# Performance work log

Hardware: AMD Instinct MI355X
Metric: run time of the kernel (lower is better)

The kernel has to match this reference:

```python
import jax, jax.numpy as jnp
import numpy as np

N_EMBED = 1024
HEAD_SIZE = 128
B, T = 8, 2048


def setup_inputs() -> dict:
    key = jax.random.key(0)
    kx, kk, kq, kv = jax.random.split(key, 4)
    x = jax.random.normal(kx, (B, T, N_EMBED), dtype=jnp.float32)
    Wk = jax.random.normal(kk, (N_EMBED, HEAD_SIZE), dtype=jnp.float32) * (N_EMBED ** -0.5)
    Wq = jax.random.normal(kq, (N_EMBED, HEAD_SIZE), dtype=jnp.float32) * (N_EMBED ** -0.5)
    Wv = jax.random.normal(kv, (N_EMBED, HEAD_SIZE), dtype=jnp.float32) * (N_EMBED ** -0.5)
    return {"x": x, "Wk": Wk, "Wq": Wq, "Wv": Wv}


def reference(x, Wk, Wq, Wv):
    # x: [B, T, C]; single-head causal attention, dropout rate 0 (identity)
    t = x.shape[1]
    k = jnp.einsum("btc,ch->bth", x, Wk)  # keys
    q = jnp.einsum("btc,ch->bth", x, Wq)  # queries
    v = jnp.einsum("btc,ch->bth", x, Wv)  # values
    scale = k.shape[-1] ** -0.5
    scores = jnp.einsum("bqh,bkh->bqk", q, k) * scale  # [B, T, T]
    causal = jnp.tril(jnp.ones((t, t), dtype=bool))
    scores = jnp.where(causal, scores, -jnp.inf)
    attn = jax.nn.softmax(scores, axis=-1)
    return jnp.einsum("bqk,bkh->bqh", attn, v)
```

## Files before the change

kernel.cpp:

```cpp
#include <hip/hip_runtime.h>
#include <hip/hip_bf16.h>
#include <math.h>

#define B_ 8
#define T_ 2048
#define C_ 1024
#define D_ 128
#define M_ (B_*T_)

typedef __attribute__((ext_vector_type(8))) short short8;
typedef __attribute__((ext_vector_type(4))) float floatx4;
typedef __hip_bfloat16 bf16;

#define QSCALE 0.12751744416218247f

#define GLDS16(gsrc, ldst) \
    __builtin_amdgcn_global_load_lds((const __attribute__((address_space(1))) unsigned int*)(gsrc), \
                                     (__attribute__((address_space(3))) unsigned int*)(ldst), 16, 0, 0)

__global__ __launch_bounds__(256) void cvt_w3_kernel(const float* __restrict__ Wq,
                                                     const float* __restrict__ Wk,
                                                     const float* __restrict__ Wv,
                                                     bf16* __restrict__ Wt2) {
    __shared__ bf16 tl[64][136];
    const int t = threadIdx.x;
    const int kc = blockIdx.x, g = blockIdx.y;
    const int k0 = kc * 64;
    const float* W = (g == 0) ? Wq : (g == 1) ? Wk : Wv;
    {
        int k = t >> 2, n0 = (t & 3) * 32;
        const float* src = W + (size_t)(k0 + k) * 128 + n0;
#pragma unroll
        for (int j = 0; j < 4; ++j) {
            float4 v0 = *(const float4*)(src + j * 8);
            float4 v1 = *(const float4*)(src + j * 8 + 4);
            union { short8 s; __hip_bfloat162 h[4]; } u;
            __hip_bfloat162 h;
            h.x = __float2bfloat16(v0.x); h.y = __float2bfloat16(v0.y); u.h[0] = h;
            h.x = __float2bfloat16(v0.z); h.y = __float2bfloat16(v0.w); u.h[1] = h;
            h.x = __float2bfloat16(v1.x); h.y = __float2bfloat16(v1.y); u.h[2] = h;
            h.x = __float2bfloat16(v1.z); h.y = __float2bfloat16(v1.w); u.h[3] = h;
            *(short8*)&tl[k][n0 + j * 8] = u.s;
        }
    }
    __syncthreads();
    {
#pragma unroll
        for (int j = 0; j < 4; ++j) {
            int cid = t + j * 256;
            int lane = cid & 63, dk = (cid >> 6) & 1, cb = cid >> 7;
            int krow = dk * 32 + (lane >> 4) * 8;
            int ncol = cb * 16 + (lane & 15);
            union { short8 s; bf16 e[8]; } u;
#pragma unroll
            for (int e = 0; e < 8; ++e) u.e[e] = tl[krow + e][ncol];
            bf16* dst = Wt2 + ((((size_t)(g * 8 + cb) * 16 + kc) * 2 + dk) * 64 + lane) * 8;
            *(short8*)dst = u.s;
        }
    }
}

__global__ __launch_bounds__(256, 2) void proj14_kernel(const float* __restrict__ x,
                                                        const bf16* __restrict__ Wt2,
                                                        bf16* __restrict__ Qb,
                                                        bf16* __restrict__ Kb,
                                                        bf16* __restrict__ Vt) {
    __shared__ __attribute__((aligned(16))) char smem[65536];
    const int t = threadIdx.x;
    const int wave = t >> 6, lane = t & 63;
    const int quad = lane >> 4, l15 = lane & 15;
    const int wr = wave >> 1, wc = wave & 1;
    const int phys = blockIdx.x;
    const int lb = (phys & 7) * 64 + (phys >> 3);
    const int rt = lb >> 1, cg = lb & 1;
    const int row0 = rt * 64;

    const bf16* wsrc[6];
#pragma unroll
    for (int j = 0; j < 6; ++j) {
        const int s = j * 4 + wave;
        const int chunkbase = (cg * 12 + (s >> 1)) * 32 + (s & 1);
        wsrc[j] = Wt2 + (size_t)chunkbase * 512 + lane * 8;
    }

    const int xwrow = t >> 2;
    const float* xbase = x + (size_t)(row0 + xwrow) * 1024 + (t & 3) * 16;
    const int xwb0 = xwrow * 128 + (((t & 3) * 32) ^ ((xwrow & 7) << 4));
    const int xwb1 = xwrow * 128 + ((((t & 3) * 32) + 16) ^ ((xwrow & 7) << 4));

    floatx4 acc[2][6];
#pragma unroll
    for (int m = 0; m < 2; ++m)
#pragma unroll
        for (int n = 0; n < 6; ++n) acc[m][n] = (floatx4)0.0f;

    float4 xr[4];

#define CVT_STORE_X(dstbase)                                                          \
    {                                                                                 \
        union { short8 s; __hip_bfloat162 h[4]; } u0, u1;                             \
        __hip_bfloat162 h;                                                            \
        h.x = __float2bfloat16(xr[0].x); h.y = __float2bfloat16(xr[0].y); u0.h[0] = h;\
        h.x = __float2bfloat16(xr[0].z); h.y = __float2bfloat16(xr[0].w); u0.h[1] = h;\
        h.x = __float2bfloat16(xr[1].x); h.y = __float2bfloat16(xr[1].y); u0.h[2] = h;\
        h.x = __float2bfloat16(xr[1].z); h.y = __float2bfloat16(xr[1].w); u0.h[3] = h;\
        h.x = __float2bfloat16(xr[2].x); h.y = __float2bfloat16(xr[2].y); u1.h[0] = h;\
        h.x = __float2bfloat16(xr[2].z); h.y = __float2bfloat16(xr[2].w); u1.h[1] = h;\
        h.x = __float2bfloat16(xr[3].x); h.y = __float2bfloat16(xr[3].y); u1.h[2] = h;\
        h.x = __float2bfloat16(xr[3].z); h.y = __float2bfloat16(xr[3].w); u1.h[3] = h;\
        *(short8*)((dstbase) + xwb0) = u0.s;                                          \
        *(short8*)((dstbase) + xwb1) = u1.s;                                          \
    }

#define COMPUTE_KC(kc_)                                                               \
    {                                                                                 \
        const char* xb = smem + 49152 + ((kc_) & 1) * 8192;                           \
        const char* wb = smem + ((kc_) & 1) * 24576;                                  \
        _Pragma("unroll")                                                             \
        for (int dk = 0; dk < 2; ++dk) {                                              \
            short8 af[2], bff[6];                                                     \
            _Pragma("unroll")                                                         \
            for (int m = 0; m < 2; ++m) {                                             \
                const int row = wr * 32 + m * 16 + l15;                               \
                const int byt = row * 128 + ((dk * 64 + quad * 16) ^ ((row & 7) << 4));\
                af[m] = *(const short8*)(xb + byt);                                   \
            }                                                                         \
            _Pragma("unroll")                                                         \
            for (int n = 0; n < 6; ++n)                                               \
                bff[n] = *(const short8*)(wb + (size_t)((wc * 6 + n) * 2 + dk) * 1024 \
                                           + lane * 16);                              \
            _Pragma("unroll")                                                         \
            for (int m = 0; m < 2; ++m)                                               \
                _Pragma("unroll")                                                     \
                for (int n = 0; n < 6; ++n)                                           \
                    acc[m][n] = __builtin_amdgcn_mfma_f32_16x16x32_bf16(af[m], bff[n],\
                                                                  acc[m][n], 0, 0, 0);\
        }                                                                             \
    }

#pragma unroll
    for (int j = 0; j < 4; ++j) xr[j] = *(const float4*)(xbase + j * 4);
    CVT_STORE_X(smem + 49152)
#pragma unroll
    for (int j = 0; j < 6; ++j)
        GLDS16(wsrc[j], smem + (j * 4 + wave) * 1024);
#pragma unroll
    for (int j = 0; j < 4; ++j) xr[j] = *(const float4*)(xbase + 64 + j * 4);

    for (int kc = 0; kc < 15; ++kc) {
        __builtin_amdgcn_s_barrier();
        {
            char* wdst = smem + ((kc + 1) & 1) * 24576;
            const size_t wko = (size_t)(kc + 1) * 1024;
#pragma unroll
            for (int j = 0; j < 6; ++j)
                GLDS16(wsrc[j] + wko, wdst + (j * 4 + wave) * 1024);
        }
        CVT_STORE_X(smem + 49152 + ((kc + 1) & 1) * 8192)
        if (kc < 14) {
#pragma unroll
            for (int j = 0; j < 4; ++j)
                xr[j] = *(const float4*)(xbase + (kc + 2) * 64 + j * 4);
        }
        asm volatile("s_waitcnt lgkmcnt(0)" ::: "memory");
        __builtin_amdgcn_s_barrier();
        __builtin_amdgcn_sched_barrier(0);
        COMPUTE_KC(kc)
    }
    __builtin_amdgcn_s_barrier();
    asm volatile("s_waitcnt vmcnt(0) lgkmcnt(0)" ::: "memory");
    __builtin_amdgcn_s_barrier();
    __builtin_amdgcn_sched_barrier(0);
    COMPUTE_KC(15)

#undef CVT_STORE_X
#undef COMPUTE_KC

    __syncthreads();
    bf16* vtl = (bf16*)smem;
#pragma unroll
    for (int m = 0; m < 2; ++m)
#pragma unroll
        for (int r = 0; r < 4; ++r) {
            const int tt = wr * 32 + m * 16 + quad * 4 + r;
            const int row = row0 + tt;
#pragma unroll
            for (int n = 0; n < 6; ++n) {
                const int colb = cg * 192 + wc * 96 + n * 16;
                const int g = colb >> 7;
                const int lc = (colb & 127) + l15;
                const float v = acc[m][n][r];
                if (g == 0)      Qb[(size_t)row * 128 + lc] = __float2bfloat16(v * QSCALE);
                else if (g == 1) Kb[(size_t)row * 128 + lc] = __float2bfloat16(v);
                else             vtl[tt * 137 + lc] = __float2bfloat16(v);
            }
        }
    if (cg == 1) {
        __syncthreads();
        int d = t >> 1, toff = (t & 1) * 32;
        union { short8 s[4]; bf16 e[32]; } u;
#pragma unroll
        for (int i = 0; i < 32; ++i) u.e[i] = vtl[(toff + i) * 137 + d];
        int bb = row0 >> 11, t0 = row0 & 2047;
        bf16* dst = Vt + (size_t)(bb * D_ + d) * T_ + t0 + toff;
#pragma unroll
        for (int j = 0; j < 4; ++j) *(short8*)(dst + j * 8) = u.s[j];
    }
}

__global__ __launch_bounds__(256, 3) void flash_fm2_kernel(const bf16* __restrict__ Qb,
                                                           const bf16* __restrict__ Kb,
                                                           const bf16* __restrict__ Vt,
                                                           float* __restrict__ out,
                                                           bf16* __restrict__ Opart,
                                                           float* __restrict__ Lpart) {
    const int tile = blockIdx.x, seg = blockIdx.y, b = blockIdx.z;
    const int keys_total = (tile + 1) * 64;
    const int nseg = (keys_total + 255) >> 8;
    if (seg >= nseg) return;

    __shared__ bf16 lds_k[64][136];
    __shared__ bf16 lds_v[128][72];
    __shared__ bf16 lds_p[4][16][72];
    const int t = threadIdx.x;
    const int wave = t >> 6, lane = t & 63;
    const int quad = lane >> 4, l15 = lane & 15;
    const int q0 = tile * 64;
    const int k_start = seg << 8;
    const int k_end = min(k_start + 256, keys_total);
    const int nch = (k_end - k_start) >> 6;

    short8 qf[4];
    {
        int qm = q0 + wave * 16 + l15;
#pragma unroll
        for (int dk = 0; dk < 4; ++dk)
            qf[dk] = *(const short8*)(Qb + (size_t)(b * T_ + qm) * 128 + dk * 32 + quad * 8);
    }

    short8 kreg[4], vreg[4];
    {
        const int k0 = k_start;
#pragma unroll
        for (int j = 0; j < 4; ++j) {
            int c = t + j * 256;
            { int r = c >> 4, co = (c & 15) * 8;
              kreg[j] = *(const short8*)(Kb + (size_t)(b * T_ + k0 + r) * 128 + co); }
            { int d = c >> 3, co = (c & 7) * 8;
              vreg[j] = *(const short8*)(Vt + (size_t)b * (D_ * T_) + d * T_ + k0 + co); }
        }
    }

    floatx4 o_acc[8];
#pragma unroll
    for (int i = 0; i < 8; ++i) o_acc[i] = (floatx4)0.0f;
    float lp[4] = {0.f, 0.f, 0.f, 0.f};
    const int qrow = q0 + wave * 16 + quad * 4;

    for (int ch = 0; ch < nch; ++ch) {
        const int k0 = k_start + (ch << 6);
        __syncthreads();
#pragma unroll
        for (int j = 0; j < 4; ++j) {
            int c = t + j * 256;
            { int r = c >> 4, co = (c & 15) * 8; *(short8*)&lds_k[r][co] = kreg[j]; }
            { int d = c >> 3, co = (c & 7) * 8;  *(short8*)&lds_v[d][co] = vreg[j]; }
        }
        if (ch + 1 < nch) {
            const int kn = k0 + 64;
#pragma unroll
            for (int j = 0; j < 4; ++j) {
                int c = t + j * 256;
                { int r = c >> 4, co = (c & 15) * 8;
                  kreg[j] = *(const short8*)(Kb + (size_t)(b * T_ + kn + r) * 128 + co); }
                { int d = c >> 3, co = (c & 7) * 8;
                  vreg[j] = *(const short8*)(Vt + (size_t)b * (D_ * T_) + d * T_ + kn + co); }
            }
        }
        __syncthreads();

        floatx4 s[4];
#pragma unroll
        for (int nt = 0; nt < 4; ++nt) s[nt] = (floatx4)0.0f;
#pragma unroll
        for (int dk = 0; dk < 4; ++dk)
#pragma unroll
            for (int nt = 0; nt < 4; ++nt) {
                short8 kb = *(const short8*)&lds_k[nt * 16 + l15][dk * 32 + quad * 8];
                s[nt] = __builtin_amdgcn_mfma_f32_16x16x32_bf16(qf[dk], kb, s[nt], 0, 0, 0);
            }

        float sv[4][4];
#pragma unroll
        for (int nt = 0; nt < 4; ++nt)
#pragma unroll
            for (int r = 0; r < 4; ++r) sv[nt][r] = s[nt][r];

        if (k0 + 63 > q0) {
#pragma unroll
            for (int nt = 0; nt < 4; ++nt) {
                int key = k0 + nt * 16 + l15;
#pragma unroll
                for (int r = 0; r < 4; ++r)
                    if (key > qrow + r) sv[nt][r] = -1e30f;
            }
        }

#pragma unroll
        for (int nt = 0; nt < 4; ++nt)
#pragma unroll
            for (int r = 0; r < 4; ++r) sv[nt][r] = exp2f(sv[nt][r]);
#pragma unroll
        for (int r = 0; r < 4; ++r)
            lp[r] += (sv[0][r] + sv[1][r]) + (sv[2][r] + sv[3][r]);

#pragma unroll
        for (int nt = 0; nt < 4; ++nt)
#pragma unroll
            for (int r = 0; r < 4; ++r)
                lds_p[wave][quad * 4 + r][nt * 16 + l15] = __float2bfloat16(sv[nt][r]);
        short8 pa0 = *(const short8*)&lds_p[wave][l15][quad * 8];
        short8 pa1 = *(const short8*)&lds_p[wave][l15][32 + quad * 8];

#pragma unroll
        for (int nt = 0; nt < 8; ++nt) {
            short8 vb0 = *(const short8*)&lds_v[nt * 16 + l15][quad * 8];
            short8 vb1 = *(const short8*)&lds_v[nt * 16 + l15][32 + quad * 8];
            o_acc[nt] = __builtin_amdgcn_mfma_f32_16x16x32_bf16(pa0, vb0, o_acc[nt], 0, 0, 0);
            o_acc[nt] = __builtin_amdgcn_mfma_f32_16x16x32_bf16(pa1, vb1, o_acc[nt], 0, 0, 0);
        }
    }

    float l_i[4];
#pragma unroll
    for (int r = 0; r < 4; ++r) {
        float v = lp[r];
        v += __shfl_xor(v, 1);
        v += __shfl_xor(v, 2);
        v += __shfl_xor(v, 4);
        v += __shfl_xor(v, 8);
        l_i[r] = v;
    }

    const int lrow = wave * 16 + quad * 4;
    if (nseg == 1) {
        float inv_l[4];
#pragma unroll
        for (int r = 0; r < 4; ++r) inv_l[r] = 1.0f / l_i[r];
#pragma unroll
        for (int f = 0; f < 8; ++f)
#pragma unroll
            for (int r = 0; r < 4; ++r)
                out[(size_t)(b * T_ + qrow + r) * 128 + f * 16 + l15] = o_acc[f][r] * inv_l[r];
    } else {
        int pre = 0;
        for (int u = 4; u < tile; ++u) pre += (u + 4) >> 2;
        const size_t slot = (size_t)b * 140 + pre + seg;
        bf16* ob = Opart + slot * (64 * 128);
#pragma unroll
        for (int f = 0; f < 8; ++f)
#pragma unroll
            for (int r = 0; r < 4; ++r)
                ob[(size_t)(lrow + r) * 128 + f * 16 + l15] = __float2bfloat16(o_acc[f][r]);
        if (l15 == 0) {
#pragma unroll
            for (int r = 0; r < 4; ++r)
                Lpart[slot * 64 + lrow + r] = l_i[r];
        }
    }
}

__global__ __launch_bounds__(256) void combine4_kernel(const bf16* __restrict__ Opart,
                                                       const float* __restrict__ Lpart,
                                                       float* __restrict__ out) {
    const int tile = blockIdx.x + 4, b = blockIdx.y;
    const int nseg = (tile + 4) >> 2;
    int pre = 0;
    for (int u = 4; u < tile; ++u) pre += (u + 4) >> 2;
    const size_t slot0 = (size_t)b * 140 + pre;
    const int t = threadIdx.x;
    const int row = t >> 2, c0 = (t & 3) * 32;

    float lsum = 0.f;
    for (int j = 0; j < nseg; ++j) lsum += Lpart[(slot0 + j) * 64 + row];

    float acc[32];
#pragma unroll
    for (int i = 0; i < 32; ++i) acc[i] = 0.f;
    for (int j = 0; j < nseg; ++j) {
        const bf16* src = Opart + (slot0 + j) * (64 * 128) + (size_t)row * 128 + c0;
#pragma unroll
        for (int u = 0; u < 4; ++u) {
            short8 v8 = *(const short8*)(src + u * 8);
#pragma unroll
            for (int e = 0; e < 8; ++e) {
                union { unsigned int u32; float f; } cv;
                cv.u32 = ((unsigned int)(unsigned short)v8[e]) << 16;
                acc[u * 8 + e] += cv.f;
            }
        }
    }
    float inv = 1.0f / lsum;
    float* dst = out + (size_t)(b * T_ + tile * 64 + row) * 128 + c0;
#pragma unroll
    for (int i = 0; i < 32; ++i) dst[i] = acc[i] * inv;
}

extern "C" void kernel_launch(void* const* d_in, const int* in_sizes, int n_in,
                              void* d_out, int out_size, void* d_ws, size_t ws_size,
                              hipStream_t stream) {
    const float* x  = (const float*)d_in[0];
    const float* Wk = (const float*)d_in[1];
    const float* Wq = (const float*)d_in[2];
    const float* Wv = (const float*)d_in[3];
    float* out = (float*)d_out;

    char* ws = (char*)d_ws;
    bf16*  Wt2   = (bf16*)ws;
    bf16*  Qb    = (bf16*)(ws + 786432);
    bf16*  Kb    = (bf16*)(ws + 4980736);
    bf16*  Vt    = (bf16*)(ws + 9175040);
    bf16*  Opart = (bf16*)(ws + 13369344);
    float* Lpart = (float*)(ws + 31719424);

    cvt_w3_kernel<<<dim3(16, 3), 256, 0, stream>>>(Wq, Wk, Wv, Wt2);
    proj14_kernel<<<512, 256, 0, stream>>>(x, Wt2, Qb, Kb, Vt);
    flash_fm2_kernel<<<dim3(32, 8, B_), 256, 0, stream>>>(Qb, Kb, Vt, out, Opart, Lpart);
    combine4_kernel<<<dim3(28, B_), 256, 0, stream>>>(Opart, Lpart, out);
}
```

Measured before the change: 82.01 us.

## Split projection into 4 column groups, read weights directly from global

The projection kernel now launches 1024 blocks, each computing 96 output columns instead of 192. It drops the LDS staging of weight tiles and instead loads MFMA B fragments straight from global or L2, since the pre-swizzled weights are small and shared by all blocks. LDS shrinks to 18KB and the occupancy hint rises to 4 blocks per CU. The V transpose epilogue is reworked for the new column split. The trade-off is that x is now read twice as many times and weight loads are uncoalesced-per-iteration global loads without double buffering.

```diff
diff --git a/kernel.cpp b/kernel.cpp
--- a/kernel.cpp
+++ b/kernel.cpp
@@ -13,10 +13,6 @@
 typedef __hip_bfloat16 bf16;
 
 #define QSCALE 0.12751744416218247f
-
-#define GLDS16(gsrc, ldst) \
-    __builtin_amdgcn_global_load_lds((const __attribute__((address_space(1))) unsigned int*)(gsrc), \
-                                     (__attribute__((address_space(3))) unsigned int*)(ldst), 16, 0, 0)
 
 __global__ __launch_bounds__(256) void cvt_w3_kernel(const float* __restrict__ Wq,
                                                      const float* __restrict__ Wk,
@@ -60,39 +56,31 @@
     }
 }
 
-__global__ __launch_bounds__(256, 2) void proj14_kernel(const float* __restrict__ x,
+__global__ __launch_bounds__(256, 4) void proj15_kernel(const float* __restrict__ x,
                                                         const bf16* __restrict__ Wt2,
                                                         bf16* __restrict__ Qb,
                                                         bf16* __restrict__ Kb,
                                                         bf16* __restrict__ Vt) {
-    __shared__ __attribute__((aligned(16))) char smem[65536];
+    __shared__ __attribute__((aligned(16))) char smem[18432];
     const int t = threadIdx.x;
     const int wave = t >> 6, lane = t & 63;
     const int quad = lane >> 4, l15 = lane & 15;
     const int wr = wave >> 1, wc = wave & 1;
     const int phys = blockIdx.x;
-    const int lb = (phys & 7) * 64 + (phys >> 3);
-    const int rt = lb >> 1, cg = lb & 1;
+    const int lb = (phys & 7) * 128 + (phys >> 3);
+    const int rt = lb >> 2, cg = lb & 3;
     const int row0 = rt * 64;
-
-    const bf16* wsrc[6];
-#pragma unroll
-    for (int j = 0; j < 6; ++j) {
-        const int s = j * 4 + wave;
-        const int chunkbase = (cg * 12 + (s >> 1)) * 32 + (s & 1);
-        wsrc[j] = Wt2 + (size_t)chunkbase * 512 + lane * 8;
-    }
 
     const int xwrow = t >> 2;
     const float* xbase = x + (size_t)(row0 + xwrow) * 1024 + (t & 3) * 16;
     const int xwb0 = xwrow * 128 + (((t & 3) * 32) ^ ((xwrow & 7) << 4));
     const int xwb1 = xwrow * 128 + ((((t & 3) * 32) + 16) ^ ((xwrow & 7) << 4));
 
-    floatx4 acc[2][6];
+    floatx4 acc[2][3];
 #pragma unroll
     for (int m = 0; m < 2; ++m)
 #pragma unroll
-        for (int n = 0; n < 6; ++n) acc[m][n] = (floatx4)0.0f;
+        for (int n = 0; n < 3; ++n) acc[m][n] = (floatx4)0.0f;
 
     float4 xr[4];
 
@@ -112,72 +100,47 @@
         *(short8*)((dstbase) + xwb1) = u1.s;                                          \
     }
 
-#define COMPUTE_KC(kc_)                                                               \
-    {                                                                                 \
-        const char* xb = smem + 49152 + ((kc_) & 1) * 8192;                           \
-        const char* wb = smem + ((kc_) & 1) * 24576;                                  \
-        _Pragma("unroll")                                                             \
-        for (int dk = 0; dk < 2; ++dk) {                                              \
-            short8 af[2], bff[6];                                                     \
-            _Pragma("unroll")                                                         \
-            for (int m = 0; m < 2; ++m) {                                             \
-                const int row = wr * 32 + m * 16 + l15;                               \
-                const int byt = row * 128 + ((dk * 64 + quad * 16) ^ ((row & 7) << 4));\
-                af[m] = *(const short8*)(xb + byt);                                   \
-            }                                                                         \
-            _Pragma("unroll")                                                         \
-            for (int n = 0; n < 6; ++n)                                               \
-                bff[n] = *(const short8*)(wb + (size_t)((wc * 6 + n) * 2 + dk) * 1024 \
-                                           + lane * 16);                              \
-            _Pragma("unroll")                                                         \
-            for (int m = 0; m < 2; ++m)                                               \
-                _Pragma("unroll")                                                     \
-                for (int n = 0; n < 6; ++n)                                           \
-                    acc[m][n] = __builtin_amdgcn_mfma_f32_16x16x32_bf16(af[m], bff[n],\
-                                                                  acc[m][n], 0, 0, 0);\
-        }                                                                             \
-    }
-
 #pragma unroll
     for (int j = 0; j < 4; ++j) xr[j] = *(const float4*)(xbase + j * 4);
-    CVT_STORE_X(smem + 49152)
-#pragma unroll
-    for (int j = 0; j < 6; ++j)
-        GLDS16(wsrc[j], smem + (j * 4 + wave) * 1024);
+    CVT_STORE_X(smem)
 #pragma unroll
     for (int j = 0; j < 4; ++j) xr[j] = *(const float4*)(xbase + 64 + j * 4);
 
-    for (int kc = 0; kc < 15; ++kc) {
-        __builtin_amdgcn_s_barrier();
-        {
-            char* wdst = smem + ((kc + 1) & 1) * 24576;
-            const size_t wko = (size_t)(kc + 1) * 1024;
-#pragma unroll
-            for (int j = 0; j < 6; ++j)
-                GLDS16(wsrc[j] + wko, wdst + (j * 4 + wave) * 1024);
-        }
-        CVT_STORE_X(smem + 49152 + ((kc + 1) & 1) * 8192)
+    for (int kc = 0; kc < 16; ++kc) {
+        __syncthreads();
+        if (kc < 15) CVT_STORE_X(smem + ((kc + 1) & 1) * 8192)
         if (kc < 14) {
 #pragma unroll
             for (int j = 0; j < 4; ++j)
                 xr[j] = *(const float4*)(xbase + (kc + 2) * 64 + j * 4);
         }
-        asm volatile("s_waitcnt lgkmcnt(0)" ::: "memory");
-        __builtin_amdgcn_s_barrier();
-        __builtin_amdgcn_sched_barrier(0);
-        COMPUTE_KC(kc)
-    }
-    __builtin_amdgcn_s_barrier();
-    asm volatile("s_waitcnt vmcnt(0) lgkmcnt(0)" ::: "memory");
-    __builtin_amdgcn_s_barrier();
-    __builtin_amdgcn_sched_barrier(0);
-    COMPUTE_KC(15)
-
+        const char* xb = smem + (kc & 1) * 8192;
+#pragma unroll
+        for (int dk = 0; dk < 2; ++dk) {
+            short8 af[2], bff[3];
+#pragma unroll
+            for (int m = 0; m < 2; ++m) {
+                const int row = wr * 32 + m * 16 + l15;
+                const int byt = row * 128 + ((dk * 64 + quad * 16) ^ ((row & 7) << 4));
+                af[m] = *(const short8*)(xb + byt);
+            }
+#pragma unroll
+            for (int n = 0; n < 3; ++n) {
+                const int cbg = cg * 6 + wc * 3 + n;
+                bff[n] = *(const short8*)(Wt2 + ((size_t)(cbg * 16 + kc) * 2 + dk) * 512 + lane * 8);
+            }
+#pragma unroll
+            for (int m = 0; m < 2; ++m)
+#pragma unroll
+                for (int n = 0; n < 3; ++n)
+                    acc[m][n] = __builtin_amdgcn_mfma_f32_16x16x32_bf16(af[m], bff[n], acc[m][n], 0, 0, 0);
+        }
+    }
 #undef CVT_STORE_X
-#undef COMPUTE_KC
 
     __syncthreads();
     bf16* vtl = (bf16*)smem;
+    const int vstride = (cg == 2) ? 40 : 104;
 #pragma unroll
     for (int m = 0; m < 2; ++m)
 #pragma unroll
@@ -185,26 +148,36 @@
             const int tt = wr * 32 + m * 16 + quad * 4 + r;
             const int row = row0 + tt;
 #pragma unroll
-            for (int n = 0; n < 6; ++n) {
-                const int colb = cg * 192 + wc * 96 + n * 16;
+            for (int n = 0; n < 3; ++n) {
+                const int colb = cg * 96 + wc * 48 + n * 16;
                 const int g = colb >> 7;
                 const int lc = (colb & 127) + l15;
                 const float v = acc[m][n][r];
                 if (g == 0)      Qb[(size_t)row * 128 + lc] = __float2bfloat16(v * QSCALE);
                 else if (g == 1) Kb[(size_t)row * 128 + lc] = __float2bfloat16(v);
-                else             vtl[tt * 137 + lc] = __float2bfloat16(v);
-            }
-        }
-    if (cg == 1) {
+                else             vtl[tt * vstride + (lc - ((cg == 2) ? 0 : 32))] = __float2bfloat16(v);
+            }
+        }
+    if (cg >= 2) {
         __syncthreads();
-        int d = t >> 1, toff = (t & 1) * 32;
-        union { short8 s[4]; bf16 e[32]; } u;
-#pragma unroll
-        for (int i = 0; i < 32; ++i) u.e[i] = vtl[(toff + i) * 137 + d];
-        int bb = row0 >> 11, t0 = row0 & 2047;
-        bf16* dst = Vt + (size_t)(bb * D_ + d) * T_ + t0 + toff;
-#pragma unroll
-        for (int j = 0; j < 4; ++j) *(short8*)(dst + j * 8) = u.s[j];
+        const int bb = row0 >> 11, t0 = row0 & 2047;
+        if (cg == 2) {
+            int d = t & 31, rowblk = t >> 5;
+            union { short8 s; bf16 e[8]; } u;
+#pragma unroll
+            for (int i = 0; i < 8; ++i) u.e[i] = vtl[(rowblk * 8 + i) * 40 + d];
+            *(short8*)(Vt + ((size_t)bb * D_ + d) * T_ + t0 + rowblk * 8) = u.s;
+        } else {
+#pragma unroll
+            for (int j = 0; j < 3; ++j) {
+                int c = t + j * 256;
+                int d = c % 96, rowblk = c / 96;
+                union { short8 s; bf16 e[8]; } u;
+#pragma unroll
+                for (int i = 0; i < 8; ++i) u.e[i] = vtl[(rowblk * 8 + i) * 104 + d];
+                *(short8*)(Vt + ((size_t)bb * D_ + 32 + d) * T_ + t0 + rowblk * 8) = u.s;
+            }
+        }
     }
 }
 
@@ -424,7 +397,7 @@
     float* Lpart = (float*)(ws + 31719424);
 
     cvt_w3_kernel<<<dim3(16, 3), 256, 0, stream>>>(Wq, Wk, Wv, Wt2);
-    proj14_kernel<<<512, 256, 0, stream>>>(x, Wt2, Qb, Kb, Vt);
+    proj15_kernel<<<1024, 256, 0, stream>>>(x, Wt2, Qb, Kb, Vt);
     flash_fm2_kernel<<<dim3(32, 8, B_), 256, 0, stream>>>(Qb, Kb, Vt, out, Opart, Lpart);
     combine4_kernel<<<dim3(28, B_), 256, 0, stream>>>(Opart, Lpart, out);
 }
```

New measurement: 92.18 us. 1.12x slower.
